# Kernel optimization log

Hardware: AMD Instinct MI355X
Metric: run time of the kernel (lower is better)

Reference implementation:

```python
import jax, jax.numpy as jnp
import numpy as np

B, S, D = 8, 4096, 64
LN_EPS = 1e-3  # keras LayerNormalization default epsilon


def setup_inputs() -> dict:
    key = jax.random.key(0)
    k1, k2 = jax.random.split(key)
    x = jax.random.normal(k1, (B, S, D), dtype=jnp.float32)
    # (D,D,D) concept tensor, scaled small like glorot-ish init
    concept_map = jax.random.normal(k2, (D, D, D), dtype=jnp.float32) * 0.02
    gamma = jnp.ones((D,), dtype=jnp.float32)
    beta = jnp.zeros((D,), dtype=jnp.float32)
    return {"x": x, "concept_map": concept_map, "gamma": gamma, "beta": beta}


def reference(x, concept_map, gamma, beta):
    b, s, d = x.shape
    # Causal Toeplitz decay matrix: T[i, j] = 1/(i-j)^2 for j < i, else 0.
    idx = jnp.arange(s)
    diff = idx[:, None] - idx[None, :]  # (S, S)
    T = jnp.where(diff > 0, 1.0 / (jnp.maximum(diff, 1).astype(x.dtype) ** 2), 0.0)
    # Weighted causal prefix sum: S_pre[b, i, c] = sum_{j<i} x[b, j, c] / (i-j)^2
    s_pre = jnp.einsum('ij,bjc->bic', T, x)
    # Bilinear form with concept tensor: out[b,i,k] = sum_{a,c} x[b,i,a] * s_pre[b,i,c] * W[k,a,c]
    outer = (x[:, :, :, None] * s_pre[:, :, None, :]).reshape(b, s, d * d)  # (B,S,D*D)
    out = outer @ concept_map.reshape(d, d * d).T  # (B,S,D)
    # Residual + LayerNorm (axis=-1, keras defaults). Dropout is identity at inference.
    r = out + x
    mu = jnp.mean(r, axis=-1, keepdims=True)
    var = jnp.mean((r - mu) ** 2, axis=-1, keepdims=True)
    y = (r - mu) / jnp.sqrt(var + LN_EPS) * gamma + beta
    return y
```

## Files before the change

kernel.cpp:

```cpp
#include <hip/hip_runtime.h>

#define S_DIM 4096
#define B_DIM 8
#define LN_EPS 1e-3f

typedef _Float16 half8 __attribute__((ext_vector_type(8)));
typedef _Float16 half2v __attribute__((ext_vector_type(2)));
typedef float f32x4 __attribute__((ext_vector_type(4)));

__global__ __launch_bounds__(256) void prep_stage1(const float* __restrict__ x,
                                                   const float* __restrict__ W,
                                                   _Float16* __restrict__ wt2,
                                                   _Float16* __restrict__ s_out) {
    if (blockIdx.x < 1024) {
        int idx = blockIdx.x * 256 + threadIdx.x;
        int a = idx >> 12;
        int j = (idx >> 9) & 7;
        int l2 = (idx >> 3) & 63;
        int e = idx & 7;
        int k = (j >> 1) * 16 + (l2 & 15);
        int c = (j & 1) * 32 + (l2 >> 4) * 8 + e;
        wt2[idx] = (_Float16)W[((k << 6) + a) * 64 + c];
        return;
    }
    const int lin = blockIdx.x - 1024;
    const int it = lin & 63;
    const int by = lin >> 6;
    const int i0 = it * 64;
    const int tid = threadIdx.x;
    const int w = tid >> 6, l = tid & 63, lg = l >> 4, lr = l & 15;

    __shared__ _Float16 Bs[64 * 72];

    f32x4 acc[4] = {};
    const float iRowF = (float)(i0 + w * 16 + lr);
    const int ldC = tid & 63;
    const int ldJ = (tid >> 6) * 16;

    const int jt0 = (it >= 2) ? (it - 2) : 0;
    for (int jt = jt0; jt <= it; ++jt) {
        const int j0 = jt * 64;
        __syncthreads();
        {
            const float* xp = x + ((size_t)by * S_DIM + j0 + ldJ) * 64 + ldC;
            half8 v0, v1;
            #pragma unroll
            for (int q = 0; q < 8; ++q) {
                v0[q] = (_Float16)xp[q * 64];
                v1[q] = (_Float16)xp[(8 + q) * 64];
            }
            *(half8*)&Bs[ldC * 72 + ldJ] = v0;
            *(half8*)&Bs[ldC * 72 + ldJ + 8] = v1;
        }
        __syncthreads();
        #pragma unroll
        for (int kk = 0; kk < 2; ++kk) {
            half8 af;
            #pragma unroll
            for (int bq = 0; bq < 8; ++bq) {
                int j = j0 + kk * 32 + lg * 8 + bq;
                float df = iRowF - (float)j;
                float tv = (df > 0.f) ? __builtin_amdgcn_rcpf(df * df) : 0.f;
                af[bq] = (_Float16)tv;
            }
            #pragma unroll
            for (int nt = 0; nt < 4; ++nt) {
                half8 bf = *(const half8*)&Bs[(nt * 16 + lr) * 72 + kk * 32 + lg * 8];
                acc[nt] = __builtin_amdgcn_mfma_f32_16x16x32_f16(af, bf, acc[nt], 0, 0, 0);
            }
        }
    }

    #pragma unroll
    for (int nt = 0; nt < 4; ++nt)
        #pragma unroll
        for (int r = 0; r < 4; ++r)
            s_out[((size_t)by * S_DIM + i0 + w * 16 + lg * 4 + r) * 64 + nt * 16 + lr]
                = (_Float16)acc[nt][r];
}

__global__ __launch_bounds__(512, 2) void stage2(const float* __restrict__ x,
                                                 const _Float16* __restrict__ s,
                                                 const _Float16* __restrict__ wt2,
                                                 const float* __restrict__ gamma,
                                                 const float* __restrict__ beta,
                                                 float* __restrict__ out) {
    const int r0 = blockIdx.x * 128;
    const int tid = threadIdx.x;
    const int w = tid >> 6, l = tid & 63, lg = l >> 4, lr = l & 15;
    const int rg = w & 1;
    const int ah = w >> 1;
    const int rbase = r0 + rg * 64;

    __shared__ __align__(16) half2v Pf[12288];

    const char* mylane = (const char*)wt2 + ((size_t)ah << 17) + l * 16;

    half8 sf[4][2];
    #pragma unroll
    for (int rt = 0; rt < 4; ++rt) {
        size_t row = (size_t)(rbase + rt * 16 + lr) * 64;
        sf[rt][0] = *(const half8*)&s[row + lg * 8];
        sf[rt][1] = *(const half8*)&s[row + 32 + lg * 8];
    }
    half8 xav[4][2];
    #pragma unroll
    for (int rt = 0; rt < 4; ++rt) {
        const float* xp = x + (size_t)(rbase + rt * 16 + lr) * 64 + ah * 16;
        half8 h0, h1;
        #pragma unroll
        for (int j = 0; j < 8; ++j) {
            h0[j] = (_Float16)xp[j];
            h1[j] = (_Float16)xp[8 + j];
        }
        xav[rt][0] = h0;
        xav[rt][1] = h1;
    }

    half8 bA[4][2], bB[4][2];

#define PREF(BUF, t_)                                                          \
    {                                                                          \
        _Pragma("unroll")                                                      \
        for (int f_ = 0; f_ < 8; ++f_)                                         \
            (&BUF[0][0])[f_] =                                                 \
                *(const half8*)(mylane + (size_t)(t_) * 8192 + f_ * 1024);     \
    }
#define CLUSTER(BUF, t_)                                                       \
    {                                                                          \
        _Pragma("unroll")                                                      \
        for (int rt_ = 0; rt_ < 4; ++rt_) {                                    \
            _Float16 xa = xav[rt_][(t_) >> 3][(t_) & 7];                       \
            half8 af0 = sf[rt_][0] * xa;                                       \
            half8 af1 = sf[rt_][1] * xa;                                       \
            _Pragma("unroll")                                                  \
            for (int nt_ = 0; nt_ < 4; ++nt_) {                                \
                acc[rt_][nt_] = __builtin_amdgcn_mfma_f32_16x16x32_f16(        \
                    af0, BUF[nt_][0], acc[rt_][nt_], 0, 0, 0);                 \
                acc[rt_][nt_] = __builtin_amdgcn_mfma_f32_16x16x32_f16(        \
                    af1, BUF[nt_][1], acc[rt_][nt_], 0, 0, 0);                 \
            }                                                                  \
        }                                                                      \
    }

    f32x4 acc[4][4] = {};
    PREF(bA, 0);
    #pragma unroll
    for (int tt = 0; tt < 8; ++tt) {
        const int t0 = tt * 2;
        PREF(bB, t0 + 1);
        CLUSTER(bA, t0);
        if (t0 + 2 < 16) PREF(bA, t0 + 2);
        CLUSTER(bB, t0 + 1);
    }
#undef PREF
#undef CLUSTER

    if (ah != 0) {
        const int q = rg * 3 + (ah - 1);
        #pragma unroll
        for (int rt = 0; rt < 4; ++rt)
            #pragma unroll
            for (int nt = 0; nt < 4; ++nt) {
                int base = (((q * 4 + rt) * 4 + nt) * 2) * 64 + l;
                half2v p01 = { (_Float16)acc[rt][nt][0], (_Float16)acc[rt][nt][1] };
                half2v p23 = { (_Float16)acc[rt][nt][2], (_Float16)acc[rt][nt][3] };
                Pf[base] = p01;
                Pf[base + 64] = p23;
            }
    }
    __syncthreads();

    if (ah == 0) {
        float gba[4], bta[4];
        #pragma unroll
        for (int nt = 0; nt < 4; ++nt) {
            gba[nt] = gamma[nt * 16 + lr];
            bta[nt] = beta[nt * 16 + lr];
        }
        #pragma unroll
        for (int rt = 0; rt < 4; ++rt) {
            float rv[4][4], sum[4], ssq[4];
            #pragma unroll
            for (int nt = 0; nt < 4; ++nt) {
                float v0 = acc[rt][nt][0], v1 = acc[rt][nt][1];
                float v2 = acc[rt][nt][2], v3 = acc[rt][nt][3];
                #pragma unroll
                for (int ph = 0; ph < 3; ++ph) {
                    int q = rg * 3 + ph;
                    int base = (((q * 4 + rt) * 4 + nt) * 2) * 64 + l;
                    half2v q01 = Pf[base];
                    half2v q23 = Pf[base + 64];
                    v0 += (float)q01[0]; v1 += (float)q01[1];
                    v2 += (float)q23[0]; v3 += (float)q23[1];
                }
                acc[rt][nt][0] = v0; acc[rt][nt][1] = v1;
                acc[rt][nt][2] = v2; acc[rt][nt][3] = v3;
            }
            #pragma unroll
            for (int reg = 0; reg < 4; ++reg) {
                const int row_l = rt * 16 + lg * 4 + reg;
                const float* xr = x + (size_t)(rbase + row_l) * 64;
                float s_ = 0.f, q_ = 0.f;
                #pragma unroll
                for (int nt = 0; nt < 4; ++nt) {
                    float v = acc[rt][nt][reg] + xr[nt * 16 + lr];
                    rv[nt][reg] = v;
                    s_ += v;
                    q_ += v * v;
                }
                sum[reg] = s_;
                ssq[reg] = q_;
            }
            #pragma unroll
            for (int m = 1; m < 16; m <<= 1) {
                #pragma unroll
                for (int reg = 0; reg < 4; ++reg) {
                    sum[reg] += __shfl_xor(sum[reg], m, 64);
                    ssq[reg] += __shfl_xor(ssq[reg], m, 64);
                }
            }
            #pragma unroll
            for (int reg = 0; reg < 4; ++reg) {
                float mean = sum[reg] * (1.f / 64.f);
                float var = ssq[reg] * (1.f / 64.f) - mean * mean;
                float rstd = __frsqrt_rn(var + LN_EPS);
                const int gr = rbase + rt * 16 + lg * 4 + reg;
                #pragma unroll
                for (int nt = 0; nt < 4; ++nt) {
                    float y = (rv[nt][reg] - mean) * rstd * gba[nt] + bta[nt];
                    out[(size_t)gr * 64 + nt * 16 + lr] = y;
                }
            }
        }
    }
}

extern "C" void kernel_launch(void* const* d_in, const int* in_sizes, int n_in,
                              void* d_out, int out_size, void* d_ws, size_t ws_size,
                              hipStream_t stream) {
    const float* x     = (const float*)d_in[0];
    const float* W     = (const float*)d_in[1];
    const float* gamma = (const float*)d_in[2];
    const float* beta  = (const float*)d_in[3];
    float* outp        = (float*)d_out;

    char* ws = (char*)d_ws;
    _Float16* s_f16 = (_Float16*)ws;
    _Float16* wt2   = (_Float16*)(ws + (size_t)B_DIM * S_DIM * 64 * 2);

    prep_stage1<<<1536, 256, 0, stream>>>(x, W, wt2, s_f16);
    stage2<<<(B_DIM * S_DIM) / 128, 512, 0, stream>>>(x, s_f16, wt2, gamma, beta, outp);
}
```

Baseline: 35.39 us.

## Split stage2 reduction dimension across eight waves with 64-row blocks

The stage2 bilinear-form kernel now uses 1024-thread blocks covering 64 rows. The 'a' reduction dimension is split across 8 wave groups of 8 values each, where before it was 4 groups of 16. Each wave holds fewer accumulators and streams half-size weight slices with finer-grained double buffering. The goal is more waves in flight for latency hiding and more blocks in the grid. The cost is a larger shared-memory partial-sum reduction (7 partials per row instead of 3) and more total weight traffic per output row.

```diff
diff --git a/kernel.cpp b/kernel.cpp
--- a/kernel.cpp
+++ b/kernel.cpp
@@ -79,90 +79,92 @@
                 = (_Float16)acc[nt][r];
 }
 
-__global__ __launch_bounds__(512, 2) void stage2(const float* __restrict__ x,
-                                                 const _Float16* __restrict__ s,
-                                                 const _Float16* __restrict__ wt2,
-                                                 const float* __restrict__ gamma,
-                                                 const float* __restrict__ beta,
-                                                 float* __restrict__ out) {
-    const int r0 = blockIdx.x * 128;
+__global__ __launch_bounds__(1024, 4) void stage2(const float* __restrict__ x,
+                                                  const _Float16* __restrict__ s,
+                                                  const _Float16* __restrict__ wt2,
+                                                  const float* __restrict__ gamma,
+                                                  const float* __restrict__ beta,
+                                                  float* __restrict__ out) {
+    const int r0 = blockIdx.x * 64;
     const int tid = threadIdx.x;
     const int w = tid >> 6, l = tid & 63, lg = l >> 4, lr = l & 15;
     const int rg = w & 1;
     const int ah = w >> 1;
-    const int rbase = r0 + rg * 64;
-
-    __shared__ __align__(16) half2v Pf[12288];
-
-    const char* mylane = (const char*)wt2 + ((size_t)ah << 17) + l * 16;
-
-    half8 sf[4][2];
+    const int rbase = r0 + rg * 32;
+
+    __shared__ __align__(16) half2v Pf[14336];
+
+    const char* mylane = (const char*)wt2 + ((size_t)ah << 16) + l * 16;
+
+    half8 sf[2][2];
+    half8 xav[2];
     #pragma unroll
-    for (int rt = 0; rt < 4; ++rt) {
-        size_t row = (size_t)(rbase + rt * 16 + lr) * 64;
-        sf[rt][0] = *(const half8*)&s[row + lg * 8];
-        sf[rt][1] = *(const half8*)&s[row + 32 + lg * 8];
-    }
-    half8 xav[4][2];
-    #pragma unroll
-    for (int rt = 0; rt < 4; ++rt) {
-        const float* xp = x + (size_t)(rbase + rt * 16 + lr) * 64 + ah * 16;
-        half8 h0, h1;
-        #pragma unroll
-        for (int j = 0; j < 8; ++j) {
-            h0[j] = (_Float16)xp[j];
-            h1[j] = (_Float16)xp[8 + j];
-        }
-        xav[rt][0] = h0;
-        xav[rt][1] = h1;
-    }
-
-    half8 bA[4][2], bB[4][2];
-
-#define PREF(BUF, t_)                                                          \
+    for (int rt = 0; rt < 2; ++rt) {
+        const size_t row = (size_t)(rbase + rt * 16 + lr);
+        sf[rt][0] = *(const half8*)&s[row * 64 + lg * 8];
+        sf[rt][1] = *(const half8*)&s[row * 64 + 32 + lg * 8];
+        const float* xp = x + row * 64 + ah * 8;
+        float4 v0 = *(const float4*)xp;
+        float4 v1 = *(const float4*)(xp + 4);
+        half8 h;
+        h[0] = (_Float16)v0.x; h[1] = (_Float16)v0.y;
+        h[2] = (_Float16)v0.z; h[3] = (_Float16)v0.w;
+        h[4] = (_Float16)v1.x; h[5] = (_Float16)v1.y;
+        h[6] = (_Float16)v1.z; h[7] = (_Float16)v1.w;
+        xav[rt] = h;
+    }
+
+    f32x4 acc[2][4] = {};
+    half8 WA[4], WB[4];
+    half8 af[2][2];
+
+#define PREFH(BUF, i_)                                                         \
     {                                                                          \
         _Pragma("unroll")                                                      \
-        for (int f_ = 0; f_ < 8; ++f_)                                         \
-            (&BUF[0][0])[f_] =                                                 \
-                *(const half8*)(mylane + (size_t)(t_) * 8192 + f_ * 1024);     \
-    }
-#define CLUSTER(BUF, t_)                                                       \
+        for (int f_ = 0; f_ < 4; ++f_)                                         \
+            BUF[f_] = *(const half8*)(mylane + (size_t)((i_) >> 1) * 8192 +    \
+                                      (((i_) & 1) * 4 + f_) * 1024);           \
+    }
+#define COMPUTEH(CB, i_)                                                       \
     {                                                                          \
-        _Pragma("unroll")                                                      \
-        for (int rt_ = 0; rt_ < 4; ++rt_) {                                    \
-            _Float16 xa = xav[rt_][(t_) >> 3][(t_) & 7];                       \
-            half8 af0 = sf[rt_][0] * xa;                                       \
-            half8 af1 = sf[rt_][1] * xa;                                       \
+        if (((i_) & 1) == 0) {                                                 \
             _Pragma("unroll")                                                  \
-            for (int nt_ = 0; nt_ < 4; ++nt_) {                                \
-                acc[rt_][nt_] = __builtin_amdgcn_mfma_f32_16x16x32_f16(        \
-                    af0, BUF[nt_][0], acc[rt_][nt_], 0, 0, 0);                 \
-                acc[rt_][nt_] = __builtin_amdgcn_mfma_f32_16x16x32_f16(        \
-                    af1, BUF[nt_][1], acc[rt_][nt_], 0, 0, 0);                 \
+            for (int rt_ = 0; rt_ < 2; ++rt_) {                                \
+                _Float16 xa_ = xav[rt_][(i_) >> 1];                            \
+                af[rt_][0] = sf[rt_][0] * xa_;                                 \
+                af[rt_][1] = sf[rt_][1] * xa_;                                 \
             }                                                                  \
         }                                                                      \
-    }
-
-    f32x4 acc[4][4] = {};
-    PREF(bA, 0);
-    #pragma unroll
-    for (int tt = 0; tt < 8; ++tt) {
-        const int t0 = tt * 2;
-        PREF(bB, t0 + 1);
-        CLUSTER(bA, t0);
-        if (t0 + 2 < 16) PREF(bA, t0 + 2);
-        CLUSTER(bB, t0 + 1);
-    }
-#undef PREF
-#undef CLUSTER
+        _Pragma("unroll")                                                      \
+        for (int rt_ = 0; rt_ < 2; ++rt_)                                      \
+            _Pragma("unroll")                                                  \
+            for (int ntl_ = 0; ntl_ < 2; ++ntl_) {                             \
+                const int nt_ = ((i_) & 1) * 2 + ntl_;                         \
+                acc[rt_][nt_] = __builtin_amdgcn_mfma_f32_16x16x32_f16(        \
+                    af[rt_][0], CB[ntl_ * 2 + 0], acc[rt_][nt_], 0, 0, 0);     \
+                acc[rt_][nt_] = __builtin_amdgcn_mfma_f32_16x16x32_f16(        \
+                    af[rt_][1], CB[ntl_ * 2 + 1], acc[rt_][nt_], 0, 0, 0);     \
+            }                                                                  \
+    }
+#define STEP(i_, CUR, NXT) { PREFH(NXT, (i_) + 1); COMPUTEH(CUR, i_); }
+
+    PREFH(WA, 0);
+    STEP(0, WA, WB);  STEP(1, WB, WA);  STEP(2, WA, WB);  STEP(3, WB, WA);
+    STEP(4, WA, WB);  STEP(5, WB, WA);  STEP(6, WA, WB);  STEP(7, WB, WA);
+    STEP(8, WA, WB);  STEP(9, WB, WA);  STEP(10, WA, WB); STEP(11, WB, WA);
+    STEP(12, WA, WB); STEP(13, WB, WA); STEP(14, WA, WB);
+    COMPUTEH(WB, 15);
+#undef PREFH
+#undef COMPUTEH
+#undef STEP
 
     if (ah != 0) {
-        const int q = rg * 3 + (ah - 1);
-        #pragma unroll
-        for (int rt = 0; rt < 4; ++rt)
+        const int q = rg * 7 + (ah - 1);
+        #pragma unroll
+        for (int rt = 0; rt < 2; ++rt)
             #pragma unroll
             for (int nt = 0; nt < 4; ++nt) {
-                int base = (((q * 4 + rt) * 4 + nt) * 2) * 64 + l;
+                int base = (((q * 2 + rt) * 4 + nt) * 2) * 64 + l;
                 half2v p01 = { (_Float16)acc[rt][nt][0], (_Float16)acc[rt][nt][1] };
                 half2v p23 = { (_Float16)acc[rt][nt][2], (_Float16)acc[rt][nt][3] };
                 Pf[base] = p01;
@@ -179,16 +181,16 @@
             bta[nt] = beta[nt * 16 + lr];
         }
         #pragma unroll
-        for (int rt = 0; rt < 4; ++rt) {
+        for (int rt = 0; rt < 2; ++rt) {
             float rv[4][4], sum[4], ssq[4];
             #pragma unroll
             for (int nt = 0; nt < 4; ++nt) {
                 float v0 = acc[rt][nt][0], v1 = acc[rt][nt][1];
                 float v2 = acc[rt][nt][2], v3 = acc[rt][nt][3];
                 #pragma unroll
-                for (int ph = 0; ph < 3; ++ph) {
-                    int q = rg * 3 + ph;
-                    int base = (((q * 4 + rt) * 4 + nt) * 2) * 64 + l;
+                for (int ph = 0; ph < 7; ++ph) {
+                    int q = rg * 7 + ph;
+                    int base = (((q * 2 + rt) * 4 + nt) * 2) * 64 + l;
                     half2v q01 = Pf[base];
                     half2v q23 = Pf[base + 64];
                     v0 += (float)q01[0]; v1 += (float)q01[1];
@@ -250,5 +252,5 @@
     _Float16* wt2   = (_Float16*)(ws + (size_t)B_DIM * S_DIM * 64 * 2);
 
     prep_stage1<<<1536, 256, 0, stream>>>(x, W, wt2, s_f16);
-    stage2<<<(B_DIM * S_DIM) / 128, 512, 0, stream>>>(x, s_f16, wt2, gamma, beta, outp);
+    stage2<<<(B_DIM * S_DIM) / 64, 1024, 0, stream>>>(x, s_f16, wt2, gamma, beta, outp);
 }
```

Measured after the change: 41.96 us. +18.6%, slower.

## Repartition stage2 waves by output column slice instead of input-a split

Applied to the files above, without the earlier changes.

Stage2 work is reassigned so each wave owns one 16-column output slice (ks) and half of the a-dimension for all 128 rows, where before each wave owned a 64-row group and a quarter of a. Only two partial sums per output are left, so the cross-wave reduction in shared memory shrinks, but the LayerNorm row statistics now have to be combined across waves through shared memory with an extra barrier. x is staged once in LDS as fp16 and read per step. The weight layout is reordered to match, and s_setprio is placed around the MFMA clusters. Each wave loads less weight data per step, at the cost of more LDS reads of x and an additional synchronization.

```diff
diff --git a/kernel.cpp b/kernel.cpp
--- a/kernel.cpp
+++ b/kernel.cpp
@@ -5,22 +5,22 @@
 #define LN_EPS 1e-3f
 
 typedef _Float16 half8 __attribute__((ext_vector_type(8)));
-typedef _Float16 half2v __attribute__((ext_vector_type(2)));
 typedef float f32x4 __attribute__((ext_vector_type(4)));
 
 __global__ __launch_bounds__(256) void prep_stage1(const float* __restrict__ x,
                                                    const float* __restrict__ W,
-                                                   _Float16* __restrict__ wt2,
+                                                   _Float16* __restrict__ wt3,
                                                    _Float16* __restrict__ s_out) {
     if (blockIdx.x < 1024) {
         int idx = blockIdx.x * 256 + threadIdx.x;
-        int a = idx >> 12;
-        int j = (idx >> 9) & 7;
+        int e  = idx & 7;
         int l2 = (idx >> 3) & 63;
-        int e = idx & 7;
-        int k = (j >> 1) * 16 + (l2 & 15);
-        int c = (j & 1) * 32 + (l2 >> 4) * 8 + e;
-        wt2[idx] = (_Float16)W[((k << 6) + a) * 64 + c];
+        int ch = (idx >> 9) & 1;
+        int ks = (idx >> 10) & 3;
+        int a  = idx >> 12;
+        int k = ks * 16 + (l2 & 15);
+        int c = ch * 32 + ((l2 >> 4) << 3) + e;
+        wt3[idx] = (_Float16)W[((k << 6) + a) * 64 + c];
         return;
     }
     const int lin = blockIdx.x - 1024;
@@ -79,158 +79,135 @@
                 = (_Float16)acc[nt][r];
 }
 
-__global__ __launch_bounds__(512, 2) void stage2(const float* __restrict__ x,
-                                                 const _Float16* __restrict__ s,
-                                                 const _Float16* __restrict__ wt2,
-                                                 const float* __restrict__ gamma,
-                                                 const float* __restrict__ beta,
-                                                 float* __restrict__ out) {
+__global__ __launch_bounds__(512) void stage2(const float* __restrict__ x,
+                                              const _Float16* __restrict__ s,
+                                              const _Float16* __restrict__ wt3,
+                                              const float* __restrict__ gamma,
+                                              const float* __restrict__ beta,
+                                              float* __restrict__ out) {
     const int r0 = blockIdx.x * 128;
     const int tid = threadIdx.x;
     const int w = tid >> 6, l = tid & 63, lg = l >> 4, lr = l & 15;
-    const int rg = w & 1;
-    const int ah = w >> 1;
-    const int rbase = r0 + rg * 64;
-
-    __shared__ __align__(16) half2v Pf[12288];
-
-    const char* mylane = (const char*)wt2 + ((size_t)ah << 17) + l * 16;
-
-    half8 sf[4][2];
+    const int ks = w & 3;
+    const int ah = w >> 2;
+
+    __shared__ __align__(16) _Float16 xT[128 * 72];
+    __shared__ __align__(16) _Float16 Pf[4][128 * 18];
+    __shared__ float Sm[4][130];
+    __shared__ float Sq[4][130];
+
+    half8 sf[8][2];
     #pragma unroll
-    for (int rt = 0; rt < 4; ++rt) {
-        size_t row = (size_t)(rbase + rt * 16 + lr) * 64;
+    for (int rt = 0; rt < 8; ++rt) {
+        const size_t row = (size_t)(r0 + rt * 16 + lr) * 64;
         sf[rt][0] = *(const half8*)&s[row + lg * 8];
         sf[rt][1] = *(const half8*)&s[row + 32 + lg * 8];
     }
-    half8 xav[4][2];
-    #pragma unroll
-    for (int rt = 0; rt < 4; ++rt) {
-        const float* xp = x + (size_t)(rbase + rt * 16 + lr) * 64 + ah * 16;
-        half8 h0, h1;
-        #pragma unroll
-        for (int j = 0; j < 8; ++j) {
-            h0[j] = (_Float16)xp[j];
-            h1[j] = (_Float16)xp[8 + j];
-        }
-        xav[rt][0] = h0;
-        xav[rt][1] = h1;
-    }
-
-    half8 bA[4][2], bB[4][2];
-
+    {
+        const int row = tid >> 2, c0 = (tid & 3) * 16;
+        const float* xp = x + (size_t)(r0 + row) * 64 + c0;
+        #pragma unroll
+        for (int hh = 0; hh < 2; ++hh) {
+            float4 v0 = *(const float4*)(xp + hh * 8);
+            float4 v1 = *(const float4*)(xp + hh * 8 + 4);
+            half8 hv;
+            hv[0] = (_Float16)v0.x; hv[1] = (_Float16)v0.y;
+            hv[2] = (_Float16)v0.z; hv[3] = (_Float16)v0.w;
+            hv[4] = (_Float16)v1.x; hv[5] = (_Float16)v1.y;
+            hv[6] = (_Float16)v1.z; hv[7] = (_Float16)v1.w;
+            *(half8*)&xT[row * 72 + c0 + hh * 8] = hv;
+        }
+    }
+    __syncthreads();
+
+    const char* mylane = (const char*)wt3 + (size_t)ks * 2048 + l * 16;
+    const size_t aBase = (size_t)ah * 32;
+
+    half8 WA[2], WB[2];
 #define PREF(BUF, t_)                                                          \
     {                                                                          \
-        _Pragma("unroll")                                                      \
-        for (int f_ = 0; f_ < 8; ++f_)                                         \
-            (&BUF[0][0])[f_] =                                                 \
-                *(const half8*)(mylane + (size_t)(t_) * 8192 + f_ * 1024);     \
-    }
+        const char* p_ = mylane + (aBase + (t_)) * 8192;                       \
+        BUF[0] = *(const half8*)(p_);                                          \
+        BUF[1] = *(const half8*)(p_ + 1024);                                   \
+    }
+
+    f32x4 acc[8] = {};
 #define CLUSTER(BUF, t_)                                                       \
     {                                                                          \
+        __builtin_amdgcn_s_setprio(1);                                         \
         _Pragma("unroll")                                                      \
-        for (int rt_ = 0; rt_ < 4; ++rt_) {                                    \
-            _Float16 xa = xav[rt_][(t_) >> 3][(t_) & 7];                       \
+        for (int rt_ = 0; rt_ < 8; ++rt_) {                                    \
+            _Float16 xa = xT[(rt_ * 16 + lr) * 72 + ah * 32 + (t_)];           \
             half8 af0 = sf[rt_][0] * xa;                                       \
             half8 af1 = sf[rt_][1] * xa;                                       \
-            _Pragma("unroll")                                                  \
-            for (int nt_ = 0; nt_ < 4; ++nt_) {                                \
-                acc[rt_][nt_] = __builtin_amdgcn_mfma_f32_16x16x32_f16(        \
-                    af0, BUF[nt_][0], acc[rt_][nt_], 0, 0, 0);                 \
-                acc[rt_][nt_] = __builtin_amdgcn_mfma_f32_16x16x32_f16(        \
-                    af1, BUF[nt_][1], acc[rt_][nt_], 0, 0, 0);                 \
-            }                                                                  \
+            acc[rt_] = __builtin_amdgcn_mfma_f32_16x16x32_f16(                 \
+                af0, BUF[0], acc[rt_], 0, 0, 0);                               \
+            acc[rt_] = __builtin_amdgcn_mfma_f32_16x16x32_f16(                 \
+                af1, BUF[1], acc[rt_], 0, 0, 0);                               \
         }                                                                      \
-    }
-
-    f32x4 acc[4][4] = {};
-    PREF(bA, 0);
+        __builtin_amdgcn_s_setprio(0);                                         \
+    }
+
+    PREF(WA, 0);
     #pragma unroll
-    for (int tt = 0; tt < 8; ++tt) {
+    for (int tt = 0; tt < 16; ++tt) {
         const int t0 = tt * 2;
-        PREF(bB, t0 + 1);
-        CLUSTER(bA, t0);
-        if (t0 + 2 < 16) PREF(bA, t0 + 2);
-        CLUSTER(bB, t0 + 1);
+        PREF(WB, t0 + 1);
+        CLUSTER(WA, t0);
+        if (t0 + 2 < 32) PREF(WA, t0 + 2);
+        CLUSTER(WB, t0 + 1);
     }
 #undef PREF
 #undef CLUSTER
 
-    if (ah != 0) {
-        const int q = rg * 3 + (ah - 1);
-        #pragma unroll
-        for (int rt = 0; rt < 4; ++rt)
-            #pragma unroll
-            for (int nt = 0; nt < 4; ++nt) {
-                int base = (((q * 4 + rt) * 4 + nt) * 2) * 64 + l;
-                half2v p01 = { (_Float16)acc[rt][nt][0], (_Float16)acc[rt][nt][1] };
-                half2v p23 = { (_Float16)acc[rt][nt][2], (_Float16)acc[rt][nt][3] };
-                Pf[base] = p01;
-                Pf[base + 64] = p23;
-            }
+    if (ah == 1) {
+        #pragma unroll
+        for (int rt = 0; rt < 8; ++rt)
+            #pragma unroll
+            for (int reg = 0; reg < 4; ++reg)
+                Pf[ks][(rt * 16 + lg * 4 + reg) * 18 + lr] = (_Float16)acc[rt][reg];
     }
     __syncthreads();
 
     if (ah == 0) {
-        float gba[4], bta[4];
-        #pragma unroll
-        for (int nt = 0; nt < 4; ++nt) {
-            gba[nt] = gamma[nt * 16 + lr];
-            bta[nt] = beta[nt * 16 + lr];
-        }
-        #pragma unroll
-        for (int rt = 0; rt < 4; ++rt) {
-            float rv[4][4], sum[4], ssq[4];
-            #pragma unroll
-            for (int nt = 0; nt < 4; ++nt) {
-                float v0 = acc[rt][nt][0], v1 = acc[rt][nt][1];
-                float v2 = acc[rt][nt][2], v3 = acc[rt][nt][3];
-                #pragma unroll
-                for (int ph = 0; ph < 3; ++ph) {
-                    int q = rg * 3 + ph;
-                    int base = (((q * 4 + rt) * 4 + nt) * 2) * 64 + l;
-                    half2v q01 = Pf[base];
-                    half2v q23 = Pf[base + 64];
-                    v0 += (float)q01[0]; v1 += (float)q01[1];
-                    v2 += (float)q23[0]; v3 += (float)q23[1];
+        #pragma unroll
+        for (int rt = 0; rt < 8; ++rt) {
+            #pragma unroll
+            for (int reg = 0; reg < 4; ++reg) {
+                const int row = rt * 16 + lg * 4 + reg;
+                float v = acc[rt][reg]
+                        + (float)Pf[ks][row * 18 + lr]
+                        + x[(size_t)(r0 + row) * 64 + ks * 16 + lr];
+                acc[rt][reg] = v;
+                float s_ = v, q_ = v * v;
+                s_ += __shfl_xor(s_, 1, 64);  q_ += __shfl_xor(q_, 1, 64);
+                s_ += __shfl_xor(s_, 2, 64);  q_ += __shfl_xor(q_, 2, 64);
+                s_ += __shfl_xor(s_, 4, 64);  q_ += __shfl_xor(q_, 4, 64);
+                s_ += __shfl_xor(s_, 8, 64);  q_ += __shfl_xor(q_, 8, 64);
+                if (lr == 0) {
+                    Sm[ks][row] = s_;
+                    Sq[ks][row] = q_;
                 }
-                acc[rt][nt][0] = v0; acc[rt][nt][1] = v1;
-                acc[rt][nt][2] = v2; acc[rt][nt][3] = v3;
-            }
+            }
+        }
+    }
+    __syncthreads();
+
+    if (ah == 0) {
+        const float gba = gamma[ks * 16 + lr];
+        const float bta = beta[ks * 16 + lr];
+        #pragma unroll
+        for (int rt = 0; rt < 8; ++rt) {
             #pragma unroll
             for (int reg = 0; reg < 4; ++reg) {
-                const int row_l = rt * 16 + lg * 4 + reg;
-                const float* xr = x + (size_t)(rbase + row_l) * 64;
-                float s_ = 0.f, q_ = 0.f;
-                #pragma unroll
-                for (int nt = 0; nt < 4; ++nt) {
-                    float v = acc[rt][nt][reg] + xr[nt * 16 + lr];
-                    rv[nt][reg] = v;
-                    s_ += v;
-                    q_ += v * v;
-                }
-                sum[reg] = s_;
-                ssq[reg] = q_;
-            }
-            #pragma unroll
-            for (int m = 1; m < 16; m <<= 1) {
-                #pragma unroll
-                for (int reg = 0; reg < 4; ++reg) {
-                    sum[reg] += __shfl_xor(sum[reg], m, 64);
-                    ssq[reg] += __shfl_xor(ssq[reg], m, 64);
-                }
-            }
-            #pragma unroll
-            for (int reg = 0; reg < 4; ++reg) {
-                float mean = sum[reg] * (1.f / 64.f);
-                float var = ssq[reg] * (1.f / 64.f) - mean * mean;
-                float rstd = __frsqrt_rn(var + LN_EPS);
-                const int gr = rbase + rt * 16 + lg * 4 + reg;
-                #pragma unroll
-                for (int nt = 0; nt < 4; ++nt) {
-                    float y = (rv[nt][reg] - mean) * rstd * gba[nt] + bta[nt];
-                    out[(size_t)gr * 64 + nt * 16 + lr] = y;
-                }
+                const int row = rt * 16 + lg * 4 + reg;
+                const float sum = Sm[0][row] + Sm[1][row] + Sm[2][row] + Sm[3][row];
+                const float ssq = Sq[0][row] + Sq[1][row] + Sq[2][row] + Sq[3][row];
+                const float mean = sum * (1.f / 64.f);
+                const float var = ssq * (1.f / 64.f) - mean * mean;
+                const float rstd = __frsqrt_rn(var + LN_EPS);
+                const float y = (acc[rt][reg] - mean) * rstd * gba + bta;
+                out[(size_t)(r0 + row) * 64 + ks * 16 + lr] = y;
             }
         }
     }
@@ -247,8 +224,8 @@
 
     char* ws = (char*)d_ws;
     _Float16* s_f16 = (_Float16*)ws;
-    _Float16* wt2   = (_Float16*)(ws + (size_t)B_DIM * S_DIM * 64 * 2);
-
-    prep_stage1<<<1536, 256, 0, stream>>>(x, W, wt2, s_f16);
-    stage2<<<(B_DIM * S_DIM) / 128, 512, 0, stream>>>(x, s_f16, wt2, gamma, beta, outp);
+    _Float16* wt3   = (_Float16*)(ws + (size_t)B_DIM * S_DIM * 64 * 2);
+
+    prep_stage1<<<1536, 256, 0, stream>>>(x, W, wt3, s_f16);
+    stage2<<<(B_DIM * S_DIM) / 128, 512, 0, stream>>>(x, s_f16, wt3, gamma, beta, outp);
 }
```

Result: slower. 43.57 us (+23.1%).
